# Optimization experiments

Hardware: AMD Instinct MI355X
Metric: run time of the kernel (lower is better)

## Reference

```python
import jax, jax.numpy as jnp
import numpy as np

EMA_DECAY = 0.99
LAPLACE_EPS = 1e-7
PERPLEXITY_EPS = 1e-10
COMMIT_COEF = 0.25


def setup_inputs() -> dict:
    key = jax.random.key(0)
    k1, k2, k3, k4 = jax.random.split(key, 4)
    B, C, T, H, W = 8, 256, 4, 32, 32
    n_codes = 2048
    z = jax.random.normal(k1, (B, C, T, H, W), dtype=jnp.float32)
    embeddings = jax.random.normal(k2, (n_codes, C), dtype=jnp.float32)
    N = jnp.ones((n_codes,), dtype=jnp.float32)  # state after _init_embeddings
    z_avg = jax.random.normal(k3, (n_codes, C), dtype=jnp.float32)
    k_rand = jax.random.normal(k4, (n_codes, C), dtype=jnp.float32)  # stand-in for randperm restart rows
    return {"z": z, "embeddings": embeddings, "N": N, "z_avg": z_avg, "k_rand": k_rand}


def reference(z, embeddings, N, z_avg, k_rand):
    b, c, t, h, w = z.shape
    n_codes = embeddings.shape[0]
    # rearrange 'b c t h w -> (b t h w) c'
    flat = jnp.transpose(z, (0, 2, 3, 4, 1)).reshape(-1, c)  # [Ntok, c]
    d2 = ((flat * flat).sum(axis=1, keepdims=True)
          - 2.0 * (flat @ embeddings.T)
          + (embeddings * embeddings).sum(axis=1)[None, :])  # [Ntok, n_codes]
    idx = jnp.argmin(d2, axis=1)  # [Ntok] int
    quant_flat = embeddings[idx]  # gather, [Ntok, c]
    # back to [b, c, t, h, w] (the double-rearrange in the torch code is a net permute back)
    quant = jnp.transpose(quant_flat.reshape(b, t, h, w, c), (0, 4, 1, 2, 3))
    commitment_loss = COMMIT_COEF * jnp.mean((z - jax.lax.stop_gradient(quant)) ** 2)
    embeddings_st = jax.lax.stop_gradient(quant - z) + z  # straight-through
    # EMA codebook update (one-hot scatter expressed as segment_sum)
    ones = jnp.ones(flat.shape[0], dtype=flat.dtype)
    counts = jax.ops.segment_sum(ones, idx, num_segments=n_codes)          # n_total
    encode_sum = jax.ops.segment_sum(flat, idx, num_segments=n_codes)      # [n_codes, c]
    new_N = N * EMA_DECAY + (1.0 - EMA_DECAY) * counts
    new_z_avg = z_avg * EMA_DECAY + (1.0 - EMA_DECAY) * encode_sum
    n = new_N.sum()
    weights = (new_N + LAPLACE_EPS) / (n + n_codes * LAPLACE_EPS) * n
    new_embeddings = new_z_avg / weights[:, None]
    usage = (new_N[:, None] >= 1.0).astype(flat.dtype)
    new_embeddings = new_embeddings * usage + k_rand * (1.0 - usage)
    # perplexity
    avg_probs = counts / flat.shape[0]
    perplexity = jnp.exp(-jnp.sum(avg_probs * jnp.log(avg_probs + PERPLEXITY_EPS)))
    encodings = idx.reshape(b, t, h, w)
    return embeddings_st, encodings, commitment_loss, perplexity, new_embeddings, new_N, new_z_avg
```

## Files before the change

kernel.cpp:

```cpp
#include <hip/hip_runtime.h>
#include <math.h>

#define NCODES 2048
#define CDIM   256
#define SPAT   4096
#define NTOK   32768
#define XSTR   260
#define EPI_TOK 32

#define ETILE    32
#define HALFCODE 1024
#define NTILES   (HALFCODE / ETILE)

typedef _Float16 half8  __attribute__((ext_vector_type(8)));
typedef float    f32x4  __attribute__((ext_vector_type(4)));

#define WS_ENORM  0
#define WS_COUNTS 2048
#define WS_LOSS   4096
#define WS_N      4097
#define WS_ESUM   4100
#define WS_IDX    528388
#define WS_OFF    561156
#define WS_CUR    563204
#define WS_SORT   565252
#define WS_SCODE  598020
#define WS_CAND   630788
#define WS_E16    761860
#define WS_XH     1024004

#define O_QUANT 0
#define O_ENC   8388608
#define O_LOSS  8421376
#define O_PERP  8421377
#define O_EMB   8421378
#define O_NN    8945666
#define O_ZAVG  8947714

__device__ inline void gl_lds16(const void* g, void* l) {
    __builtin_amdgcn_global_load_lds(
        (const __attribute__((address_space(1))) void*)g,
        (__attribute__((address_space(3))) void*)l, 16, 0, 0);
}

__device__ inline unsigned umn(unsigned a, unsigned b) { return a < b ? a : b; }
__device__ inline unsigned umx(unsigned a, unsigned b) { return a > b ? a : b; }
__device__ inline unsigned shflx16(unsigned v, int off) {
    return (unsigned)__shfl_xor((int)v, off, 16);
}

__global__ void k_ecvt(const float* __restrict__ emb, float* __restrict__ ws) {
    const int tid  = threadIdx.x;
    const int code = (blockIdx.x << 3) + (tid >> 5);
    const int cg   = tid & 31;
    const float* src = emb + (size_t)code * CDIM + (cg << 3);
    const float4 f0 = *(const float4*)src;
    const float4 f1 = *(const float4*)(src + 4);
    half8 h = { (_Float16)f0.x, (_Float16)f0.y, (_Float16)f0.z, (_Float16)f0.w,
                (_Float16)f1.x, (_Float16)f1.y, (_Float16)f1.z, (_Float16)f1.w };
    char* dst = (char*)(ws + WS_E16) + (size_t)code * 512 + ((cg ^ (code & 7)) << 4);
    *(half8*)dst = h;
    float s = f0.x * f0.x + f0.y * f0.y + f0.z * f0.z + f0.w * f0.w
            + f1.x * f1.x + f1.y * f1.y + f1.z * f1.z + f1.w * f1.w;
#pragma unroll
    for (int off = 16; off; off >>= 1) s += __shfl_down(s, off, 32);
    if (cg == 0) ws[WS_ENORM + code] = s;
}

__global__ __launch_bounds__(128, 4) void k_main(
    const float* __restrict__ z, float* __restrict__ ws)
{
    __shared__ half8 Es8[2][ETILE][32];

    const int tid = threadIdx.x;
    const int raw = blockIdx.x;
    const int xcd = raw & 7, sub = raw >> 3;
    const int tb  = xcd * 64 + (sub >> 1);
    const int ch  = sub & 1;
    const int b   = tb >> 6;
    const int s0  = (tb & 63) * 64;
    const float* zb = z + (size_t)b * CDIM * SPAT + s0;
    const char* e16g = (const char*)(ws + WS_E16) + (size_t)ch * HALFCODE * 512;

    const int l  = tid & 63, w = tid >> 6;
    const int lr = l & 15, lg = l >> 4;

    {
        char* dst = (char*)&Es8[0][0][0];
#pragma unroll
        for (int q = 0; q < 8; ++q) {
            const int off = ((q << 1) + w) << 10;
            gl_lds16(e16g + off + (l << 4), dst + off);
        }
    }

    half8 a[2][8];
#pragma unroll
    for (int as = 0; as < 2; ++as)
#pragma unroll
    for (int ks = 0; ks < 8; ++ks) {
        float v[8];
#pragma unroll
        for (int e = 0; e < 8; ++e)
            v[e] = zb[(size_t)(ks * 32 + lg * 8 + e) * SPAT + (w * 32 + as * 16 + lr)];
        half8 h = { (_Float16)v[0], (_Float16)v[1], (_Float16)v[2], (_Float16)v[3],
                    (_Float16)v[4], (_Float16)v[5], (_Float16)v[6], (_Float16)v[7] };
        a[as][ks] = h;
    }

    if (ch == 0) {
        _Float16* xh = (_Float16*)(ws + WS_XH);
#pragma unroll
        for (int as = 0; as < 2; ++as) {
            _Float16* xr = xh + (size_t)(b * SPAT + s0 + w * 32 + as * 16 + lr) * CDIM;
#pragma unroll
            for (int ks = 0; ks < 8; ++ks)
                *(half8*)(xr + ks * 32 + lg * 8) = a[as][ks];
        }
    }

    unsigned kb0[2][4], kb1[2][4];
#pragma unroll
    for (int as = 0; as < 2; ++as)
#pragma unroll
    for (int r = 0; r < 4; ++r) { kb0[as][r] = 0xFFFFFFFFu; kb1[as][r] = 0xFFFFFFFFu; }

    __syncthreads();

    int p = 0;
    for (int tile = 0; tile < NTILES; ++tile) {
        if (tile < NTILES - 1) {
            const char* src = e16g + (size_t)(tile + 1) * (ETILE * 512);
            char* dst = (char*)&Es8[p ^ 1][0][0];
#pragma unroll
            for (int q = 0; q < 8; ++q) {
                const int off = ((q << 1) + w) << 10;
                gl_lds16(src + off + (l << 4), dst + off);
            }
        }

        const float en0 = ws[WS_ENORM + ch * HALFCODE + tile * ETILE + lr];
        const float en1 = ws[WS_ENORM + ch * HALFCODE + tile * ETILE + 16 + lr];

        f32x4 acc[2][2];
#pragma unroll
        for (int as = 0; as < 2; ++as)
#pragma unroll
        for (int j = 0; j < 2; ++j) acc[as][j] = (f32x4)0.0f;

        half8 bf0[2], bf1[2];
#pragma unroll
        for (int j = 0; j < 2; ++j) {
            const int row = j * 16 + lr;
            bf0[j] = Es8[p][row][lg ^ (row & 7)];
        }
#pragma unroll
        for (int ks = 0; ks < 8; ++ks) {
            if (ks < 7) {
#pragma unroll
                for (int j = 0; j < 2; ++j) {
                    const int row = j * 16 + lr;
                    if (ks & 1) bf0[j] = Es8[p][row][((ks + 1) * 4 + lg) ^ (row & 7)];
                    else        bf1[j] = Es8[p][row][((ks + 1) * 4 + lg) ^ (row & 7)];
                }
            }
            __builtin_amdgcn_s_setprio(1);
#pragma unroll
            for (int as = 0; as < 2; ++as)
#pragma unroll
            for (int j = 0; j < 2; ++j)
                acc[as][j] = __builtin_amdgcn_mfma_f32_16x16x32_f16(
                    a[as][ks], (ks & 1) ? bf1[j] : bf0[j], acc[as][j], 0, 0, 0);
            __builtin_amdgcn_s_setprio(0);
        }

        const float enb0 = en0 + 4096.0f;
        const float enb1 = en1 + 4096.0f;
        const unsigned code0 = (unsigned)(ch * HALFCODE + tile * ETILE + lr);
        const unsigned code1 = code0 + 16u;
#pragma unroll
        for (int as = 0; as < 2; ++as)
#pragma unroll
        for (int r = 0; r < 4; ++r) {
            {
                const float d = fmaf(acc[as][0][r], -2.0f, enb0);
                const unsigned key = (__float_as_uint(d) & 0xFFFFF800u) | code0;
                const unsigned hi = umx(kb0[as][r], key);
                kb0[as][r] = umn(kb0[as][r], key);
                kb1[as][r] = umn(kb1[as][r], hi);
            }
            {
                const float d = fmaf(acc[as][1][r], -2.0f, enb1);
                const unsigned key = (__float_as_uint(d) & 0xFFFFF800u) | code1;
                const unsigned hi = umx(kb0[as][r], key);
                kb0[as][r] = umn(kb0[as][r], key);
                kb1[as][r] = umn(kb1[as][r], hi);
            }
        }

        __syncthreads();
        p ^= 1;
    }

#pragma unroll
    for (int as = 0; as < 2; ++as)
#pragma unroll
    for (int r = 0; r < 4; ++r) {
        unsigned k0 = kb0[as][r], k1 = kb1[as][r];
        unsigned k2 = 0xFFFFFFFFu, k3 = 0xFFFFFFFFu;
#pragma unroll
        for (int off = 8; off; off >>= 1) {
            const unsigned o0 = shflx16(k0, off);
            const unsigned o1 = shflx16(k1, off);
            const unsigned o2 = shflx16(k2, off);
            const unsigned o3 = shflx16(k3, off);
            const unsigned m0 = umn(k0, o3), m1 = umn(k1, o2);
            const unsigned m2 = umn(k2, o1), m3 = umn(k3, o0);
            const unsigned t0 = umn(m0, m2), t2 = umx(m0, m2);
            const unsigned t1 = umn(m1, m3), t3 = umx(m1, m3);
            k0 = umn(t0, t1); k1 = umx(t0, t1);
            k2 = umn(t2, t3); k3 = umx(t2, t3);
        }
        if (lr == 0) {
            const int tokg = b * SPAT + s0 + w * 32 + as * 16 + lg * 4 + r;
            ushort4 c4;
            c4.x = (unsigned short)(k0 & 2047u);
            c4.y = (unsigned short)(k1 & 2047u);
            c4.z = (unsigned short)(k2 & 2047u);
            c4.w = (unsigned short)(k3 & 2047u);
            *(ushort4*)((unsigned short*)((int*)ws + WS_CAND) + (size_t)tokg * 8 + ch * 4) = c4;
        }
    }
}

__global__ __launch_bounds__(256, 4) void k_epi(
    const float* __restrict__ z, const float* __restrict__ emb,
    float* __restrict__ ws, float* __restrict__ out)
{
    __shared__ float Xs[EPI_TOK * XSTR];
    __shared__ int   idxs[EPI_TOK];
    __shared__ float lloss[EPI_TOK];

    const int tid = threadIdx.x, blk = blockIdx.x;
    const int b   = blk >> 7;
    const int s0  = (blk & 127) * EPI_TOK;
    const float* zb = z + (size_t)b * CDIM * SPAT + s0;

    {
        const int s  = tid & 31;
        const int c0 = tid >> 5;
#pragma unroll 4
        for (int c = c0; c < CDIM; c += 8)
            Xs[s * XSTR + c] = zb[(size_t)c * SPAT + s];
    }
    __syncthreads();

    {
        const int t = tid >> 3, h = tid & 7;
        const unsigned short* cp =
            (const unsigned short*)((int*)ws + WS_CAND) + ((size_t)blk * EPI_TOK + t) * 8;
        const int mycand = cp[h];
        const float en_h = ws[WS_ENORM + mycand];

        int cand[8];
        {
            const ushort4 ca = *(const ushort4*)cp;
            const ushort4 cb = *(const ushort4*)(cp + 4);
            cand[0] = ca.x; cand[1] = ca.y; cand[2] = ca.z; cand[3] = ca.w;
            cand[4] = cb.x; cand[5] = cb.y; cand[6] = cb.z; cand[7] = cb.w;
        }

        float4 xq[8];
#pragma unroll
        for (int q = 0; q < 8; ++q)
            xq[q] = *(const float4*)&Xs[t * XSTR + q * 32 + h * 4];

        float xn = 0.0f;
#pragma unroll
        for (int q = 0; q < 8; ++q)
            xn += xq[q].x * xq[q].x + xq[q].y * xq[q].y
                + xq[q].z * xq[q].z + xq[q].w * xq[q].w;
        xn += __shfl_xor(xn, 1, 8);
        xn += __shfl_xor(xn, 2, 8);
        xn += __shfl_xor(xn, 4, 8);

        float p8[8];
#pragma unroll
        for (int k = 0; k < 8; ++k) {
            const float* er = emb + (size_t)cand[k] * CDIM + h * 4;
            float dp = 0.0f;
#pragma unroll
            for (int q = 0; q < 8; ++q) {
                const float4 e4 = *(const float4*)(er + q * 32);
                dp += xq[q].x * e4.x + xq[q].y * e4.y + xq[q].z * e4.z + xq[q].w * e4.w;
            }
            p8[k] = dp;
        }

        float np4[4];
#pragma unroll
        for (int k2 = 0; k2 < 4; ++k2) {
            const float own = (h & 1) ? p8[2 * k2 + 1] : p8[2 * k2];
            const float snd = (h & 1) ? p8[2 * k2]     : p8[2 * k2 + 1];
            np4[k2] = own + __shfl_xor(snd, 1, 8);
        }
        float nq2[2];
#pragma unroll
        for (int k3 = 0; k3 < 2; ++k3) {
            const float own = ((h >> 1) & 1) ? np4[2 * k3 + 1] : np4[2 * k3];
            const float snd = ((h >> 1) & 1) ? np4[2 * k3]     : np4[2 * k3 + 1];
            nq2[k3] = own + __shfl_xor(snd, 2, 8);
        }
        const float own = ((h >> 2) & 1) ? nq2[1] : nq2[0];
        const float snd = ((h >> 2) & 1) ? nq2[0] : nq2[1];
        const float dot = own + __shfl_xor(snd, 4, 8);

        float bd = en_h - 2.0f * dot;
        int   bi = mycand;
#pragma unroll
        for (int off = 4; off; off >>= 1) {
            const float od = __shfl_xor(bd, off, 8);
            const int   oi = __shfl_xor(bi, off, 8);
            if (od < bd || (od == bd && oi < bi)) { bd = od; bi = oi; }
        }
        if (h == 0) {
            idxs[t]  = bi;
            lloss[t] = xn + bd;
            out[O_ENC + blk * EPI_TOK + t] = (float)bi;
            ((int*)ws)[WS_IDX + blk * EPI_TOK + t] = bi;
            atomicAdd(ws + WS_COUNTS + bi, 1.0f);
        }
    }
    __syncthreads();

    {
        const int t = tid >> 3, h = tid & 7;
        const float* ewin = emb + (size_t)idxs[t] * CDIM + h * 4;
#pragma unroll
        for (int q = 0; q < 8; ++q)
            *(float4*)&Xs[t * XSTR + q * 32 + h * 4] = *(const float4*)(ewin + q * 32);
    }
    __syncthreads();

    {
        const int s  = tid & 31;
        const int c0 = tid >> 5;
        float* qcol = out + O_QUANT + (size_t)b * CDIM * SPAT + s0 + s;
#pragma unroll 4
        for (int c = c0; c < CDIM; c += 8)
            qcol[(size_t)c * SPAT] = Xs[s * XSTR + c];
    }
    if (tid == 0) {
        float ls = 0.0f;
#pragma unroll
        for (int t = 0; t < EPI_TOK; ++t) ls += lloss[t];
        atomicAdd(ws + WS_LOSS, ls);
    }
}

__global__ void k_finalize(const float* __restrict__ Nin, float* __restrict__ ws,
                           float* __restrict__ out) {
    __shared__ float r1[4], r2[4];
    __shared__ int   wsum[4];
    const int tid  = threadIdx.x;
    const int base = tid * 8;

    float cnt[8];
    {
        const float4 c0 = *(const float4*)(ws + WS_COUNTS + base);
        const float4 c1 = *(const float4*)(ws + WS_COUNTS + base + 4);
        cnt[0] = c0.x; cnt[1] = c0.y; cnt[2] = c0.z; cnt[3] = c0.w;
        cnt[4] = c1.x; cnt[5] = c1.y; cnt[6] = c1.z; cnt[7] = c1.w;
    }

    float nsum = 0.0f, H = 0.0f;
    int   tsum = 0;
#pragma unroll
    for (int j = 0; j < 8; ++j) {
        const float cf = cnt[j];
        const float nn = Nin[base + j] * 0.99f + 0.01f * cf;
        out[O_NN + base + j] = nn;
        nsum += nn;
        const float p = cf * (1.0f / 32768.0f);
        H += p * logf(p + 1e-10f);
        tsum += (int)cf;
    }

    int inc = tsum;
#pragma unroll
    for (int off = 1; off < 64; off <<= 1) {
        const int v = __shfl_up(inc, off, 64);
        if ((tid & 63) >= off) inc += v;
    }
    const int wv = tid >> 6, ln = tid & 63;
    if (ln == 63) wsum[wv] = inc;

#pragma unroll
    for (int off = 32; off; off >>= 1) {
        nsum += __shfl_down(nsum, off);
        H    += __shfl_down(H, off);
    }
    if (ln == 0) { r1[wv] = nsum; r2[wv] = H; }
    __syncthreads();

    int wbase = 0;
    for (int q = 0; q < wv; ++q) wbase += wsum[q];
    int run = wbase + inc - tsum;
    int* offp = (int*)ws + WS_OFF;
    int* curp = (int*)ws + WS_CUR;
#pragma unroll
    for (int j = 0; j < 8; ++j) {
        offp[base + j] = run;
        curp[base + j] = run;
        run += (int)cnt[j];
    }

    if (tid == 0) {
        const float nt = r1[0] + r1[1] + r1[2] + r1[3];
        const float Ht = r2[0] + r2[1] + r2[2] + r2[3];
        ws[WS_N] = nt;
        out[O_PERP] = expf(-Ht);
        out[O_LOSS] = 0.25f * ws[WS_LOSS] * (1.0f / 8388608.0f);
    }
}

__global__ void k_scatter(float* __restrict__ ws) {
    const int t    = blockIdx.x * 256 + threadIdx.x;
    const int code = ((const int*)ws)[WS_IDX + t];
    const int slot = atomicAdd((int*)ws + WS_CUR + code, 1);
    ((int*)ws)[WS_SORT  + slot] = t;
    ((int*)ws)[WS_SCODE + slot] = code;
}

__global__ __launch_bounds__(256) void k_gather(float* __restrict__ ws) {
    __shared__ int stok[64], scod[64];
    const int g = blockIdx.x, tid = threadIdx.x, c = tid;
    if (tid < 64) {
        stok[tid] = ((const int*)ws)[WS_SORT  + g * 64 + tid];
        scod[tid] = ((const int*)ws)[WS_SCODE + g * 64 + tid];
    }
    __syncthreads();

    const _Float16* xh = (const _Float16*)(ws + WS_XH);
    float* esum = ws + WS_ESUM;

    float acc = 0.0f;
    for (int k0 = 0; k0 < 64; k0 += 8) {
        float v[8];
#pragma unroll
        for (int j = 0; j < 8; ++j)
            v[j] = (float)xh[(size_t)stok[k0 + j] * CDIM + c];
#pragma unroll
        for (int j = 0; j < 8; ++j) {
            const int k = k0 + j;
            acc += v[j];
            if (k == 63 || scod[k] != scod[k + 1]) {
                atomicAdd(&esum[(size_t)scod[k] * CDIM + c], acc);
                acc = 0.0f;
            }
        }
    }
}

__global__ __launch_bounds__(256) void k_update(
    const float* __restrict__ zavg, const float* __restrict__ krand,
    const float* __restrict__ ws, float* __restrict__ out)
{
    const int i = blockIdx.x, c = threadIdx.x;
    const float nn  = out[O_NN + i];
    const float n   = ws[WS_N];
    const float wgt = (nn + 1e-7f) / (n + NCODES * 1e-7f) * n;
    const size_t o  = (size_t)i * CDIM + c;
    const float ez  = 0.99f * zavg[o] + 0.01f * ws[WS_ESUM + o];
    out[O_ZAVG + o] = ez;
    out[O_EMB + o]  = (nn >= 1.0f) ? (ez / wgt) : krand[o];
}

extern "C" void kernel_launch(void* const* d_in, const int* in_sizes, int n_in,
                              void* d_out, int out_size, void* d_ws, size_t ws_size,
                              hipStream_t stream) {
    const float* z     = (const float*)d_in[0];
    const float* emb   = (const float*)d_in[1];
    const float* Nin   = (const float*)d_in[2];
    const float* zavg  = (const float*)d_in[3];
    const float* krand = (const float*)d_in[4];
    float* out = (float*)d_out;
    float* ws  = (float*)d_ws;

    hipMemsetAsync(ws + WS_COUNTS, 0,
                   (size_t)(2048 + 4 + NCODES * CDIM) * sizeof(float), stream);

    k_ecvt    <<<NCODES / 8,  256, 0, stream>>>(emb, ws);
    k_main    <<<1024,        128, 0, stream>>>(z, ws);
    k_epi     <<<1024,        256, 0, stream>>>(z, emb, ws, out);
    k_finalize<<<1,           256, 0, stream>>>(Nin, ws, out);
    k_scatter <<<NTOK / 256,  256, 0, stream>>>(ws);
    k_gather  <<<NTOK / 64,   256, 0, stream>>>(ws);
    k_update  <<<NCODES,      256, 0, stream>>>(zavg, krand, ws, out);
}
```

Measured before the change: 138.1 us.

## Load codebook fragments directly into registers, drop LDS staging in main kernel

The codebook fp16 image is rewritten in MFMA fragment order so each lane can load its B operand straight from global memory. The main distance kernel drops the LDS double buffer and its barriers, prefetching fragments two k-steps ahead into registers. Blocks shrink to a single wave of 32 tokens and twice as many blocks are launched. This removes LDS traffic and block syncs, but every wave now reads the full half-codebook from L2 on its own, with no sharing between waves.

```diff
diff --git a/kernel.cpp b/kernel.cpp
--- a/kernel.cpp
+++ b/kernel.cpp
@@ -11,6 +11,7 @@
 #define ETILE    32
 #define HALFCODE 1024
 #define NTILES   (HALFCODE / ETILE)
+#define HALFBYTES 524288
 
 typedef _Float16 half8  __attribute__((ext_vector_type(8)));
 typedef float    f32x4  __attribute__((ext_vector_type(4)));
@@ -37,12 +38,6 @@
 #define O_NN    8945666
 #define O_ZAVG  8947714
 
-__device__ inline void gl_lds16(const void* g, void* l) {
-    __builtin_amdgcn_global_load_lds(
-        (const __attribute__((address_space(1))) void*)g,
-        (__attribute__((address_space(3))) void*)l, 16, 0, 0);
-}
-
 __device__ inline unsigned umn(unsigned a, unsigned b) { return a < b ? a : b; }
 __device__ inline unsigned umx(unsigned a, unsigned b) { return a > b ? a : b; }
 __device__ inline unsigned shflx16(unsigned v, int off) {
@@ -58,7 +53,15 @@
     const float4 f1 = *(const float4*)(src + 4);
     half8 h = { (_Float16)f0.x, (_Float16)f0.y, (_Float16)f0.z, (_Float16)f0.w,
                 (_Float16)f1.x, (_Float16)f1.y, (_Float16)f1.z, (_Float16)f1.w };
-    char* dst = (char*)(ws + WS_E16) + (size_t)code * 512 + ((cg ^ (code & 7)) << 4);
+    const int half = code >> 10;
+    const int cih  = code & 1023;
+    const int tile = cih >> 5;
+    const int j    = (cih >> 4) & 1;
+    const int lr   = cih & 15;
+    const int ks   = cg >> 2;
+    const int lg   = cg & 3;
+    char* dst = (char*)(ws + WS_E16) + (size_t)half * HALFBYTES
+              + (size_t)((((tile * 8 + ks) * 2 + j) * 64) + (lg * 16 + lr)) * 16;
     *(half8*)dst = h;
     float s = f0.x * f0.x + f0.y * f0.y + f0.z * f0.z + f0.w * f0.w
             + f1.x * f1.x + f1.y * f1.y + f1.z * f1.z + f1.w * f1.w;
@@ -67,32 +70,25 @@
     if (cg == 0) ws[WS_ENORM + code] = s;
 }
 
-__global__ __launch_bounds__(128, 4) void k_main(
+__global__ __launch_bounds__(64, 2) void k_main(
     const float* __restrict__ z, float* __restrict__ ws)
 {
-    __shared__ half8 Es8[2][ETILE][32];
-
-    const int tid = threadIdx.x;
+    const int l   = threadIdx.x;
     const int raw = blockIdx.x;
     const int xcd = raw & 7, sub = raw >> 3;
-    const int tb  = xcd * 64 + (sub >> 1);
+    const int tb  = xcd * 128 + (sub >> 1);
     const int ch  = sub & 1;
-    const int b   = tb >> 6;
-    const int s0  = (tb & 63) * 64;
+    const int b   = tb >> 7;
+    const int s0  = (tb & 127) * 32;
     const float* zb = z + (size_t)b * CDIM * SPAT + s0;
-    const char* e16g = (const char*)(ws + WS_E16) + (size_t)ch * HALFCODE * 512;
-
-    const int l  = tid & 63, w = tid >> 6;
+    const char* eimg = (const char*)(ws + WS_E16) + (size_t)ch * HALFBYTES;
+
     const int lr = l & 15, lg = l >> 4;
 
-    {
-        char* dst = (char*)&Es8[0][0][0];
-#pragma unroll
-        for (int q = 0; q < 8; ++q) {
-            const int off = ((q << 1) + w) << 10;
-            gl_lds16(e16g + off + (l << 4), dst + off);
-        }
-    }
+    half8 c0 = *(const half8*)(eimg + 0 * 1024 + l * 16);
+    half8 c1 = *(const half8*)(eimg + 1 * 1024 + l * 16);
+    half8 d0 = *(const half8*)(eimg + 2 * 1024 + l * 16);
+    half8 d1 = *(const half8*)(eimg + 3 * 1024 + l * 16);
 
     half8 a[2][8];
 #pragma unroll
@@ -102,7 +98,7 @@
         float v[8];
 #pragma unroll
         for (int e = 0; e < 8; ++e)
-            v[e] = zb[(size_t)(ks * 32 + lg * 8 + e) * SPAT + (w * 32 + as * 16 + lr)];
+            v[e] = zb[(size_t)(ks * 32 + lg * 8 + e) * SPAT + (as * 16 + lr)];
         half8 h = { (_Float16)v[0], (_Float16)v[1], (_Float16)v[2], (_Float16)v[3],
                     (_Float16)v[4], (_Float16)v[5], (_Float16)v[6], (_Float16)v[7] };
         a[as][ks] = h;
@@ -112,7 +108,7 @@
         _Float16* xh = (_Float16*)(ws + WS_XH);
 #pragma unroll
         for (int as = 0; as < 2; ++as) {
-            _Float16* xr = xh + (size_t)(b * SPAT + s0 + w * 32 + as * 16 + lr) * CDIM;
+            _Float16* xr = xh + (size_t)(b * SPAT + s0 + as * 16 + lr) * CDIM;
 #pragma unroll
             for (int ks = 0; ks < 8; ++ks)
                 *(half8*)(xr + ks * 32 + lg * 8) = a[as][ks];
@@ -125,20 +121,7 @@
 #pragma unroll
     for (int r = 0; r < 4; ++r) { kb0[as][r] = 0xFFFFFFFFu; kb1[as][r] = 0xFFFFFFFFu; }
 
-    __syncthreads();
-
-    int p = 0;
     for (int tile = 0; tile < NTILES; ++tile) {
-        if (tile < NTILES - 1) {
-            const char* src = e16g + (size_t)(tile + 1) * (ETILE * 512);
-            char* dst = (char*)&Es8[p ^ 1][0][0];
-#pragma unroll
-            for (int q = 0; q < 8; ++q) {
-                const int off = ((q << 1) + w) << 10;
-                gl_lds16(src + off + (l << 4), dst + off);
-            }
-        }
-
         const float en0 = ws[WS_ENORM + ch * HALFCODE + tile * ETILE + lr];
         const float en1 = ws[WS_ENORM + ch * HALFCODE + tile * ETILE + 16 + lr];
 
@@ -148,30 +131,26 @@
 #pragma unroll
         for (int j = 0; j < 2; ++j) acc[as][j] = (f32x4)0.0f;
 
-        half8 bf0[2], bf1[2];
-#pragma unroll
-        for (int j = 0; j < 2; ++j) {
-            const int row = j * 16 + lr;
-            bf0[j] = Es8[p][row][lg ^ (row & 7)];
-        }
 #pragma unroll
         for (int ks = 0; ks < 8; ++ks) {
-            if (ks < 7) {
-#pragma unroll
-                for (int j = 0; j < 2; ++j) {
-                    const int row = j * 16 + lr;
-                    if (ks & 1) bf0[j] = Es8[p][row][((ks + 1) * 4 + lg) ^ (row & 7)];
-                    else        bf1[j] = Es8[p][row][((ks + 1) * 4 + lg) ^ (row & 7)];
-                }
+            const int step = tile * 8 + ks;
+            half8 n0, n1;
+            if (step + 2 < 256) {
+                const char* p = eimg + (size_t)(step + 2) * 2048 + l * 16;
+                n0 = *(const half8*)p;
+                n1 = *(const half8*)(p + 1024);
             }
             __builtin_amdgcn_s_setprio(1);
 #pragma unroll
-            for (int as = 0; as < 2; ++as)
-#pragma unroll
-            for (int j = 0; j < 2; ++j)
-                acc[as][j] = __builtin_amdgcn_mfma_f32_16x16x32_f16(
-                    a[as][ks], (ks & 1) ? bf1[j] : bf0[j], acc[as][j], 0, 0, 0);
+            for (int as = 0; as < 2; ++as) {
+                acc[as][0] = __builtin_amdgcn_mfma_f32_16x16x32_f16(
+                    a[as][ks], c0, acc[as][0], 0, 0, 0);
+                acc[as][1] = __builtin_amdgcn_mfma_f32_16x16x32_f16(
+                    a[as][ks], c1, acc[as][1], 0, 0, 0);
+            }
             __builtin_amdgcn_s_setprio(0);
+            c0 = d0; c1 = d1;
+            if (step + 2 < 256) { d0 = n0; d1 = n1; }
         }
 
         const float enb0 = en0 + 4096.0f;
@@ -197,9 +176,6 @@
                 kb1[as][r] = umn(kb1[as][r], hi);
             }
         }
-
-        __syncthreads();
-        p ^= 1;
     }
 
 #pragma unroll
@@ -222,7 +198,7 @@
             k2 = umn(t2, t3); k3 = umx(t2, t3);
         }
         if (lr == 0) {
-            const int tokg = b * SPAT + s0 + w * 32 + as * 16 + lg * 4 + r;
+            const int tokg = b * SPAT + s0 + as * 16 + lg * 4 + r;
             ushort4 c4;
             c4.x = (unsigned short)(k0 & 2047u);
             c4.y = (unsigned short)(k1 & 2047u);
@@ -491,7 +467,7 @@
                    (size_t)(2048 + 4 + NCODES * CDIM) * sizeof(float), stream);
 
     k_ecvt    <<<NCODES / 8,  256, 0, stream>>>(emb, ws);
-    k_main    <<<1024,        128, 0, stream>>>(z, ws);
+    k_main    <<<2048,        64,  0, stream>>>(z, ws);
     k_epi     <<<1024,        256, 0, stream>>>(z, emb, ws, out);
     k_finalize<<<1,           256, 0, stream>>>(Nin, ws, out);
     k_scatter <<<NTOK / 256,  256, 0, stream>>>(ws);
```

New measurement: 136.0 us, median of 3. No clear change (-1.6%).
